# Optimization experiments

Hardware: AMD Instinct MI355X
Metric: run time of the kernel (lower is better)

The kernel has to match this reference:

```python
import jax, jax.numpy as jnp
import numpy as np

N, D_TOK, K = 8192, 256, 16


def knn_idx(xyz, k):
    # squared pairwise distances, diagonal excluded (loop=False)
    sq = jnp.sum(xyz * xyz, axis=-1)                      # [N]
    dist = sq[:, None] - 2.0 * (xyz @ xyz.T) + sq[None, :]  # [N,N]
    dist = dist + jnp.eye(xyz.shape[0], dtype=xyz.dtype) * jnp.asarray(1e10, xyz.dtype)
    _, idx = jax.lax.top_k(-dist, k)                      # [N,k] nearest neighbors j for each target i
    return idx


def edgeconv(x, nbr, W1, b1, W2, b2):
    # EdgeConv message: nn(concat(x_i, x_j - x_i)), aggr = max over neighbors
    n, d = x.shape
    k = nbr.shape[1]
    xi = x[:, None, :]                                    # [N,1,D]
    xj = x[nbr]                                           # [N,k,D] gather
    msg = jnp.concatenate([jnp.broadcast_to(xi, (n, k, d)), xj - xi], axis=-1)  # [N,k,2D]
    h = jax.nn.relu(msg @ W1 + b1) @ W2 + b2              # [N,k,token_dim]
    return jnp.max(h, axis=1)                             # [N,token_dim]


def setup_inputs() -> dict:
    key = jax.random.key(0)
    ks = jax.random.split(key, 10)
    d_in = 2 * (D_TOK + 3)
    s1 = 1.0 / np.sqrt(d_in)
    s2 = 1.0 / np.sqrt(D_TOK)
    return {
        "xyz": jax.random.normal(ks[0], (N, 3), dtype=jnp.float32),
        "feat": jax.random.normal(ks[1], (N, D_TOK), dtype=jnp.float32),
        "W1a": jax.random.normal(ks[2], (d_in, D_TOK), dtype=jnp.float32) * s1,
        "b1a": jnp.zeros((D_TOK,), dtype=jnp.float32),
        "W2a": jax.random.normal(ks[3], (D_TOK, D_TOK), dtype=jnp.float32) * s2,
        "b2a": jnp.zeros((D_TOK,), dtype=jnp.float32),
        "W1b": jax.random.normal(ks[4], (d_in, D_TOK), dtype=jnp.float32) * s1,
        "b1b": jnp.zeros((D_TOK,), dtype=jnp.float32),
        "W2b": jax.random.normal(ks[5], (D_TOK, D_TOK), dtype=jnp.float32) * s2,
        "b2b": jnp.zeros((D_TOK,), dtype=jnp.float32),
    }


def reference(xyz, feat, W1a, b1a, W2a, b2a, W1b, b1b, W2b, b2b):
    nbr = knn_idx(xyz, K)                                 # [N,k], built once, reused by both convs
    x = jnp.concatenate([feat, xyz], axis=-1)             # [N, D_TOK+3]
    x = edgeconv(x, nbr, W1a, b1a, W2a, b2a)              # [N, D_TOK]
    x = jnp.concatenate([x, xyz], axis=-1)                # [N, D_TOK+3]
    x = edgeconv(x, nbr, W1b, b1b, W2b, b2b)              # [N, D_TOK]
    return x
```

## Files before the change

kernel.cpp:

```cpp
#include <hip/hip_runtime.h>
#include <cfloat>

#define N_PTS 8192
#define DTOK 256
#define KNN 16

typedef __attribute__((ext_vector_type(8))) short short8;
typedef __attribute__((ext_vector_type(4))) float float4v;
typedef __attribute__((ext_vector_type(2))) float float2v;

__device__ inline short f2bf(float f) {
  unsigned u = __float_as_uint(f);
  u += 0x7fffu + ((u >> 16) & 1u);
  return (short)(u >> 16);
}
__device__ inline float bf2f(short h) {
  return __uint_as_float(((unsigned)(unsigned short)h) << 16);
}

__device__ inline float2v pk_mul(float2v a, float2v b) {
  float2v d;
  asm("v_pk_mul_f32 %0, %1, %2" : "=v"(d) : "v"(a), "v"(b));
  return d;
}
__device__ inline float2v pk_fma(float2v a, float2v b, float2v c) {
  float2v d;
  asm("v_pk_fma_f32 %0, %1, %2, %3" : "=v"(d) : "v"(a), "v"(b), "v"(c));
  return d;
}
__device__ inline float2v pk_add(float2v a, float2v b) {
  float2v d;
  asm("v_pk_add_f32 %0, %1, %2" : "=v"(d) : "v"(a), "v"(b));
  return d;
}

__global__ __launch_bounds__(256) void knn_prep_kernel(
    const float* __restrict__ xyz, float4* __restrict__ xyz4) {
  const int i = blockIdx.x * 256 + threadIdx.x;
  float x = xyz[3 * i], y = xyz[3 * i + 1], z = xyz[3 * i + 2];
  float sq = __fadd_rn(__fadd_rn(__fmul_rn(x, x), __fmul_rn(y, y)),
                       __fmul_rn(z, z));
  xyz4[i] = make_float4(x, y, z, sq);
}

__device__ inline void insert_group(float d, int base, float t, int lane,
                                    float& sd, int& sj, float& s15) {
  unsigned long long m = __ballot(d <= t);
  while (m) {
    const int src = __ffsll(m) - 1;
    m &= m - 1;
    const float dc = __shfl(d, src);
    if (dc < s15) {
      const int jc = base + src;
      const unsigned long long bm = __ballot(sd <= dc) & 0xFFFFull;
      const int pos = (int)__popcll(bm);
      const float pu = __shfl_up(sd, 1);
      const int ju = __shfl_up(sj, 1);
      if (lane < 16) {
        if (lane > pos)        { sd = pu; sj = ju; }
        else if (lane == pos)  { sd = dc; sj = jc; }
      }
      s15 = __shfl(sd, 15);
    }
  }
}

#define KCH 512
#define NCH (N_PTS / KCH)

__global__ __launch_bounds__(256) void knn_select_kernel(
    const float4* __restrict__ xyz4, int* __restrict__ nbr) {
  __shared__ float4 sA[2][4][64];
  __shared__ float4 sB[2][4][64];
  const int tid = threadIdx.x;
  const int lane = tid & 63;
  const int wave = tid >> 6;
  const int i0 = blockIdx.x * 8 + wave * 2;
  const int i1 = i0 + 1;

  const float4 q0 = xyz4[i0];
  const float4 q1 = xyz4[i1];
  const float2v x02 = {q0.x, q0.x}, y02 = {q0.y, q0.y};
  const float2v z02 = {q0.z, q0.z}, s02 = {q0.w, q0.w};
  const float2v x12 = {q1.x, q1.x}, y12 = {q1.y, q1.y};
  const float2v z12 = {q1.z, q1.z}, s12 = {q1.w, q1.w};
  const float2v n2 = {-2.0f, -2.0f};

  const int ib128 = i0 & ~127;
  const int ih0 = (i0 >> 6) & 1, il0 = i0 & 63;
  const int ih1 = (i1 >> 6) & 1, il1 = i1 & 63;

  const int sgj = wave * 128 + lane;

  {
    const float4 c0 = xyz4[sgj];
    const float4 c1 = xyz4[sgj + 64];
    sA[0][wave][lane] = make_float4(c0.x, c1.x, c0.y, c1.y);
    sB[0][wave][lane] = make_float4(c0.z, c1.z, c0.w, c1.w);
  }
  __syncthreads();

  float a00 = FLT_MAX, a01 = FLT_MAX, a10 = FLT_MAX, a11 = FLT_MAX;
  for (int c = 0; c < NCH; ++c) {
    const int b = c & 1;
    float4 nx0, nx1;
    if (c < NCH - 1) {
      nx0 = xyz4[(c + 1) * KCH + sgj];
      nx1 = xyz4[(c + 1) * KCH + sgj + 64];
    }
    const int cbase = c * KCH;
    #pragma unroll
    for (int ps = 0; ps < 4; ++ps) {
      const float4 a = sA[b][ps][lane];
      const float4 bb = sB[b][ps][lane];
      const float2v px = {a.x, a.y}, py = {a.z, a.w};
      const float2v pz = {bb.x, bb.y}, pw = {bb.z, bb.w};
      const bool selfg = (cbase + ps * 128 == ib128);
      const float2v dot0 =
          pk_fma(z02, pz, pk_fma(y02, py, pk_mul(x02, px)));
      float2v d0 = pk_add(pk_fma(n2, dot0, s02), pw);
      const float2v dot1 =
          pk_fma(z12, pz, pk_fma(y12, py, pk_mul(x12, px)));
      float2v d1 = pk_add(pk_fma(n2, dot1, s12), pw);
      if (selfg) {
        if (lane == il0) {
          if (ih0) d0.y = __fadd_rn(d0.y, 1e10f);
          else     d0.x = __fadd_rn(d0.x, 1e10f);
        }
        if (lane == il1) {
          if (ih1) d1.y = __fadd_rn(d1.y, 1e10f);
          else     d1.x = __fadd_rn(d1.x, 1e10f);
        }
      }
      a00 = fminf(a00, d0.x);
      a01 = fminf(a01, d0.y);
      a10 = fminf(a10, d1.x);
      a11 = fminf(a11, d1.y);
    }
    if (c < NCH - 1) {
      sA[b ^ 1][wave][lane] = make_float4(nx0.x, nx1.x, nx0.y, nx1.y);
      sB[b ^ 1][wave][lane] = make_float4(nx0.z, nx1.z, nx0.w, nx1.w);
    }
    __syncthreads();
  }

  float v0 = fminf(a00, a01);
  float v1 = fminf(a10, a11);
  #pragma unroll
  for (int k = 2; k <= 64; k <<= 1) {
    #pragma unroll
    for (int j = k >> 1; j > 0; j >>= 1) {
      const float o0 = __shfl_xor(v0, j, 64);
      const float o1 = __shfl_xor(v1, j, 64);
      const bool keepmin = ((lane & k) == 0) == ((lane & j) == 0);
      v0 = keepmin ? fminf(v0, o0) : fmaxf(v0, o0);
      v1 = keepmin ? fminf(v1, o1) : fmaxf(v1, o1);
    }
  }
  const float t0 = __shfl(v0, 15, 64);
  const float t1 = __shfl(v1, 15, 64);

  float sd0 = FLT_MAX, sd1 = FLT_MAX;
  int sj0 = 0, sj1 = 0;
  float s150 = FLT_MAX, s151 = FLT_MAX;

  const int gself = i0 >> 6;

  float4 pc = xyz4[lane];
  #pragma unroll 2
  for (int grp = 0; grp < N_PTS / 64; ++grp) {
    float4 pn;
    if (grp < N_PTS / 64 - 1) pn = xyz4[(grp + 1) * 64 + lane];

    const float dot0 = fmaf(q0.z, pc.z, fmaf(q0.y, pc.y,
                                             __fmul_rn(q0.x, pc.x)));
    float d0 = __fadd_rn(__fmaf_rn(-2.0f, dot0, q0.w), pc.w);
    const float dot1 = fmaf(q1.z, pc.z, fmaf(q1.y, pc.y,
                                             __fmul_rn(q1.x, pc.x)));
    float d1 = __fadd_rn(__fmaf_rn(-2.0f, dot1, q1.w), pc.w);
    if (grp == gself) {
      if (lane == il0) d0 = __fadd_rn(d0, 1e10f);
      if (lane == il1) d1 = __fadd_rn(d1, 1e10f);
    }

    insert_group(d0, grp * 64, t0, lane, sd0, sj0, s150);
    insert_group(d1, grp * 64, t1, lane, sd1, sj1, s151);
    pc = pn;
  }

  if (lane < 16) {
    nbr[i0 * KNN + lane] = sj0;
    nbr[i1 * KNN + lane] = sj1;
  }
}

__global__ __launch_bounds__(256) void convert_w_kernel(
    const float* __restrict__ W1, short* __restrict__ bhi,
    short* __restrict__ blo) {
  const int n = blockIdx.x;
  const int k = threadIdx.x;
  const float v = (n < 256) ? W1[k * DTOK + n]
                            : W1[(259 + k) * DTOK + (n - 256)];
  short h = f2bf(v);
  bhi[n * 256 + k] = h;
  blo[n * 256 + k] = f2bf(v - bf2f(h));
}

__global__ __launch_bounds__(256, 2) void pq_gemm_fused_kernel(
    const float* __restrict__ A, const short* __restrict__ Bthi,
    const short* __restrict__ Btlo, const float* __restrict__ xyz,
    const float* __restrict__ W1, const float* __restrict__ b1,
    float* __restrict__ R, float* __restrict__ Q) {
  __shared__ short Ahi[64][32], Alo[64][32];
  __shared__ short Bhi[128][32], Blo[128][32];
  __shared__ float Qs[64][65];
  __shared__ float sx[64][3];
  __shared__ float swz[6][64];
  __shared__ float sb1[64];

  const int tid = threadIdx.x;
  const int lane = tid & 63;
  const int wave = tid >> 6;
  const int l15 = lane & 15;
  const int quad = lane >> 4;
  const int mh = wave & 1;
  const int qh = wave >> 1;
  const int m0 = blockIdx.x * 64;
  const int np0 = blockIdx.y * 64;

  if (tid < 64) {
    sx[tid][0] = xyz[(m0 + tid) * 3];
    sx[tid][1] = xyz[(m0 + tid) * 3 + 1];
    sx[tid][2] = xyz[(m0 + tid) * 3 + 2];
  } else if (tid < 128) {
    int n = tid - 64;
    sb1[n] = b1[np0 + n];
    #pragma unroll
    for (int r = 0; r < 3; ++r) {
      swz[r][n] = W1[(256 + r) * DTOK + np0 + n];
      swz[3 + r][n] = W1[(515 + r) * DTOK + np0 + n];
    }
  }

  float4v acc[2][4];
  #pragma unroll
  for (int mf = 0; mf < 2; ++mf)
    #pragma unroll
    for (int nf = 0; nf < 4; ++nf)
      #pragma unroll
      for (int e = 0; e < 4; ++e) acc[mf][nf][e] = 0.f;

  const int ar = tid >> 2;
  const int ak = (tid & 3) * 8;

  #pragma unroll 1
  for (int kc = 0; kc < 8; ++kc) {
    const int k0 = kc * 32;
    __syncthreads();
    {
      const float* asrc = A + (size_t)(m0 + ar) * 256 + k0 + ak;
      float4 a0 = *(const float4*)asrc;
      float4 a1 = *(const float4*)(asrc + 4);
      float v[8] = {a0.x, a0.y, a0.z, a0.w, a1.x, a1.y, a1.z, a1.w};
      short8 h8, l8;
      #pragma unroll
      for (int e = 0; e < 8; ++e) {
        short h = f2bf(v[e]);
        h8[e] = h;
        l8[e] = f2bf(v[e] - bf2f(h));
      }
      *(short8*)(&Ahi[ar][ak]) = h8;
      *(short8*)(&Alo[ar][ak]) = l8;
    }
    #pragma unroll
    for (int l = 0; l < 4; ++l) {
      const int rem = tid + 256 * (l & 1);
      const int row = rem >> 2;
      const int koff = (rem & 3) * 8;
      const int n = (row < 64) ? (np0 + row) : (256 + np0 + row - 64);
      const short* src = ((l < 2) ? Bthi : Btlo) + (size_t)n * 256 + k0 + koff;
      short8 vv = *(const short8*)src;
      if (l < 2) *(short8*)(&Bhi[row][koff]) = vv;
      else       *(short8*)(&Blo[row][koff]) = vv;
    }
    __syncthreads();

    short8 ah[2], al[2], bh[4], bl[4];
    #pragma unroll
    for (int mf = 0; mf < 2; ++mf) {
      ah[mf] = *(const short8*)(&Ahi[mh * 32 + mf * 16 + l15][quad * 8]);
      al[mf] = *(const short8*)(&Alo[mh * 32 + mf * 16 + l15][quad * 8]);
    }
    #pragma unroll
    for (int nf = 0; nf < 4; ++nf) {
      bh[nf] = *(const short8*)(&Bhi[qh * 64 + nf * 16 + l15][quad * 8]);
      bl[nf] = *(const short8*)(&Blo[qh * 64 + nf * 16 + l15][quad * 8]);
    }
    #pragma unroll
    for (int mf = 0; mf < 2; ++mf)
      #pragma unroll
      for (int nf = 0; nf < 4; ++nf) {
        acc[mf][nf] = __builtin_amdgcn_mfma_f32_16x16x32_bf16(
            ah[mf], bh[nf], acc[mf][nf], 0, 0, 0);
        acc[mf][nf] = __builtin_amdgcn_mfma_f32_16x16x32_bf16(
            ah[mf], bl[nf], acc[mf][nf], 0, 0, 0);
        acc[mf][nf] = __builtin_amdgcn_mfma_f32_16x16x32_bf16(
            al[mf], bh[nf], acc[mf][nf], 0, 0, 0);
      }
  }

  if (qh == 1) {
    #pragma unroll
    for (int mf = 0; mf < 2; ++mf)
      #pragma unroll
      for (int nf = 0; nf < 4; ++nf)
        #pragma unroll
        for (int e = 0; e < 4; ++e) {
          int row = mh * 32 + mf * 16 + quad * 4 + e;
          int col = nf * 16 + l15;
          float q = acc[mf][nf][e] + sx[row][0] * swz[3][col] +
                    sx[row][1] * swz[4][col] + sx[row][2] * swz[5][col];
          Qs[row][col] = q;
          Q[(size_t)(m0 + row) * DTOK + np0 + col] = q;
        }
  }
  __syncthreads();
  if (qh == 0) {
    #pragma unroll
    for (int mf = 0; mf < 2; ++mf)
      #pragma unroll
      for (int nf = 0; nf < 4; ++nf)
        #pragma unroll
        for (int e = 0; e < 4; ++e) {
          int row = mh * 32 + mf * 16 + quad * 4 + e;
          int col = nf * 16 + l15;
          float p = acc[mf][nf][e] + sx[row][0] * swz[0][col] +
                    sx[row][1] * swz[1][col] + sx[row][2] * swz[2][col];
          R[(size_t)(m0 + row) * DTOK + np0 + col] =
              (p + sb1[col]) - Qs[row][col];
        }
  }
}

#define EP 8

__global__ __launch_bounds__(256, 2) void edge_mfma_kernel(
    const float* __restrict__ R, const float* __restrict__ Q,
    const int* __restrict__ nbr, const float* __restrict__ W2,
    const float* __restrict__ b2, float* __restrict__ out,
    int num_groups, int groups_per_block) {
  __shared__ short Hs[EP * KNN * DTOK];
  const int lane = threadIdx.x & 63;
  const int wave = threadIdx.x >> 6;
  const int l15 = lane & 15;
  const int quad = lane >> 4;

  short8 bfr[4][8];
  #pragma unroll
  for (int nt_i = 0; nt_i < 4; ++nt_i) {
    const int n = (wave * 4 + nt_i) * 16 + l15;
    #pragma unroll
    for (int kt = 0; kt < 8; ++kt) {
      short8 f;
      #pragma unroll
      for (int jj = 0; jj < 8; ++jj) {
        int k = kt * 32 + quad * 8 + jj;
        f[jj] = f2bf(W2[k * DTOK + n]);
      }
      bfr[nt_i][kt] = f;
    }
  }

  const int wc8 = lane >> 1;
  const int wsub = (lane & 1) * 4;

  for (int gi = 0; gi < groups_per_block; ++gi) {
    const int g = blockIdx.x + gi * gridDim.x;
    if (g >= num_groups) break;
    const int i0 = g * EP;

    {
      const int ia = i0 + wave * 2;
      const int jr0 = nbr[ia * KNN + l15];
      const int jr1 = nbr[(ia + 1) * KNN + l15];
      const float4 ri0 = ((const float4*)(R + (size_t)ia * DTOK))[lane];
      const float4 ri1 = ((const float4*)(R + (size_t)(ia + 1) * DTOK))[lane];
      #pragma unroll
      for (int pp = 0; pp < 2; ++pp) {
        const float4 ri = pp ? ri1 : ri0;
        const int jr = pp ? jr1 : jr0;
        #pragma unroll
        for (int k = 0; k < KNN; ++k) {
          const int j = __shfl(jr, k, 16);
          const float4 qj = ((const float4*)(Q + (size_t)j * DTOK))[lane];
          const int r = wave * 32 + pp * 16 + k;
          uint2 pk;
          pk.x = ((unsigned)(unsigned short)f2bf(fmaxf(ri.x + qj.x, 0.f))) |
                 (((unsigned)(unsigned short)f2bf(fmaxf(ri.y + qj.y, 0.f))) << 16);
          pk.y = ((unsigned)(unsigned short)f2bf(fmaxf(ri.z + qj.z, 0.f))) |
                 (((unsigned)(unsigned short)f2bf(fmaxf(ri.w + qj.w, 0.f))) << 16);
          *(uint2*)(&Hs[r * DTOK + ((wc8 ^ (r & 7)) << 3) + wsub]) = pk;
        }
      }
    }
    __syncthreads();

    #pragma unroll
    for (int mp = 0; mp < 4; ++mp) {
      float4v acc[2][4];
      #pragma unroll
      for (int mi = 0; mi < 2; ++mi)
        #pragma unroll
        for (int nt_i = 0; nt_i < 4; ++nt_i)
          #pragma unroll
          for (int e = 0; e < 4; ++e) acc[mi][nt_i][e] = 0.f;

      #pragma unroll
      for (int kt = 0; kt < 8; ++kt) {
        const int pc = ((kt * 4 + quad) ^ (l15 & 7)) << 3;
        const short8 a0 = *(const short8*)(
            &Hs[((mp * 2 + 0) * 16 + l15) * DTOK + pc]);
        const short8 a1 = *(const short8*)(
            &Hs[((mp * 2 + 1) * 16 + l15) * DTOK + pc]);
        #pragma unroll
        for (int nt_i = 0; nt_i < 4; ++nt_i) {
          acc[0][nt_i] = __builtin_amdgcn_mfma_f32_16x16x32_bf16(
              a0, bfr[nt_i][kt], acc[0][nt_i], 0, 0, 0);
          acc[1][nt_i] = __builtin_amdgcn_mfma_f32_16x16x32_bf16(
              a1, bfr[nt_i][kt], acc[1][nt_i], 0, 0, 0);
        }
      }

      #pragma unroll
      for (int mi = 0; mi < 2; ++mi) {
        #pragma unroll
        for (int nt_i = 0; nt_i < 4; ++nt_i) {
          float rm = fmaxf(fmaxf(acc[mi][nt_i][0], acc[mi][nt_i][1]),
                           fmaxf(acc[mi][nt_i][2], acc[mi][nt_i][3]));
          rm = fmaxf(rm, __shfl_xor(rm, 16, 64));
          rm = fmaxf(rm, __shfl_xor(rm, 32, 64));
          if (lane < 16) {
            const int i = i0 + mp * 2 + mi;
            const int n = (wave * 4 + nt_i) * 16 + lane;
            out[(size_t)i * DTOK + n] = rm + b2[n];
          }
        }
      }
    }
    __syncthreads();
  }
}

extern "C" void kernel_launch(void* const* d_in, const int* in_sizes, int n_in,
                              void* d_out, int out_size, void* d_ws,
                              size_t ws_size, hipStream_t stream) {
  const float* xyz = (const float*)d_in[0];
  const float* feat = (const float*)d_in[1];
  const float* W1a = (const float*)d_in[2];
  const float* b1a = (const float*)d_in[3];
  const float* W2a = (const float*)d_in[4];
  const float* b2a = (const float*)d_in[5];
  const float* W1b = (const float*)d_in[6];
  const float* b1b = (const float*)d_in[7];
  const float* W2b = (const float*)d_in[8];
  const float* b2b = (const float*)d_in[9];
  float* out = (float*)d_out;

  char* w = (char*)d_ws;
  const size_t SZ_NBR = (size_t)N_PTS * KNN * sizeof(int);
  const size_t MB = 1024 * 1024;
  int* nbr = (int*)w;
  char* w1 = w + SZ_NBR;
  float4* xyz4 = (float4*)w1;
  float* R = (float*)(w1 + 8 * MB);
  float* Q = (float*)(w + SZ_NBR + 16 * MB);
  short* Bthi = (short*)(w + SZ_NBR + 24 * MB);
  short* Btlo = Bthi + 512 * 256;
  float* bufC = out;

  knn_prep_kernel<<<N_PTS / 256, 256, 0, stream>>>(xyz, xyz4);
  knn_select_kernel<<<N_PTS / 8, 256, 0, stream>>>(xyz4, nbr);

  const int num_groups = N_PTS / EP;
  const int nblocks = 512;

  convert_w_kernel<<<512, 256, 0, stream>>>(W1a, Bthi, Btlo);
  pq_gemm_fused_kernel<<<dim3(N_PTS / 64, 4), 256, 0, stream>>>(
      feat, Bthi, Btlo, xyz, W1a, b1a, R, Q);
  edge_mfma_kernel<<<nblocks, 256, 0, stream>>>(R, Q, nbr, W2a, b2a, bufC,
                                                num_groups, 2);

  convert_w_kernel<<<512, 256, 0, stream>>>(W1b, Bthi, Btlo);
  pq_gemm_fused_kernel<<<dim3(N_PTS / 64, 4), 256, 0, stream>>>(
      bufC, Bthi, Btlo, xyz, W1b, b1b, R, Q);
  edge_mfma_kernel<<<nblocks, 256, 0, stream>>>(R, Q, nbr, W2b, b2b, out,
                                                num_groups, 2);
}
```

Measured before the change: 229.7 us.

## Fuse kNN selection and first P/Q GEMM into one heterogeneous kernel launch

```diff
diff --git a/kernel.cpp b/kernel.cpp
--- a/kernel.cpp
+++ b/kernel.cpp
@@ -65,135 +65,6 @@
   }
 }
 
-#define KCH 512
-#define NCH (N_PTS / KCH)
-
-__global__ __launch_bounds__(256) void knn_select_kernel(
-    const float4* __restrict__ xyz4, int* __restrict__ nbr) {
-  __shared__ float4 sA[2][4][64];
-  __shared__ float4 sB[2][4][64];
-  const int tid = threadIdx.x;
-  const int lane = tid & 63;
-  const int wave = tid >> 6;
-  const int i0 = blockIdx.x * 8 + wave * 2;
-  const int i1 = i0 + 1;
-
-  const float4 q0 = xyz4[i0];
-  const float4 q1 = xyz4[i1];
-  const float2v x02 = {q0.x, q0.x}, y02 = {q0.y, q0.y};
-  const float2v z02 = {q0.z, q0.z}, s02 = {q0.w, q0.w};
-  const float2v x12 = {q1.x, q1.x}, y12 = {q1.y, q1.y};
-  const float2v z12 = {q1.z, q1.z}, s12 = {q1.w, q1.w};
-  const float2v n2 = {-2.0f, -2.0f};
-
-  const int ib128 = i0 & ~127;
-  const int ih0 = (i0 >> 6) & 1, il0 = i0 & 63;
-  const int ih1 = (i1 >> 6) & 1, il1 = i1 & 63;
-
-  const int sgj = wave * 128 + lane;
-
-  {
-    const float4 c0 = xyz4[sgj];
-    const float4 c1 = xyz4[sgj + 64];
-    sA[0][wave][lane] = make_float4(c0.x, c1.x, c0.y, c1.y);
-    sB[0][wave][lane] = make_float4(c0.z, c1.z, c0.w, c1.w);
-  }
-  __syncthreads();
-
-  float a00 = FLT_MAX, a01 = FLT_MAX, a10 = FLT_MAX, a11 = FLT_MAX;
-  for (int c = 0; c < NCH; ++c) {
-    const int b = c & 1;
-    float4 nx0, nx1;
-    if (c < NCH - 1) {
-      nx0 = xyz4[(c + 1) * KCH + sgj];
-      nx1 = xyz4[(c + 1) * KCH + sgj + 64];
-    }
-    const int cbase = c * KCH;
-    #pragma unroll
-    for (int ps = 0; ps < 4; ++ps) {
-      const float4 a = sA[b][ps][lane];
-      const float4 bb = sB[b][ps][lane];
-      const float2v px = {a.x, a.y}, py = {a.z, a.w};
-      const float2v pz = {bb.x, bb.y}, pw = {bb.z, bb.w};
-      const bool selfg = (cbase + ps * 128 == ib128);
-      const float2v dot0 =
-          pk_fma(z02, pz, pk_fma(y02, py, pk_mul(x02, px)));
-      float2v d0 = pk_add(pk_fma(n2, dot0, s02), pw);
-      const float2v dot1 =
-          pk_fma(z12, pz, pk_fma(y12, py, pk_mul(x12, px)));
-      float2v d1 = pk_add(pk_fma(n2, dot1, s12), pw);
-      if (selfg) {
-        if (lane == il0) {
-          if (ih0) d0.y = __fadd_rn(d0.y, 1e10f);
-          else     d0.x = __fadd_rn(d0.x, 1e10f);
-        }
-        if (lane == il1) {
-          if (ih1) d1.y = __fadd_rn(d1.y, 1e10f);
-          else     d1.x = __fadd_rn(d1.x, 1e10f);
-        }
-      }
-      a00 = fminf(a00, d0.x);
-      a01 = fminf(a01, d0.y);
-      a10 = fminf(a10, d1.x);
-      a11 = fminf(a11, d1.y);
-    }
-    if (c < NCH - 1) {
-      sA[b ^ 1][wave][lane] = make_float4(nx0.x, nx1.x, nx0.y, nx1.y);
-      sB[b ^ 1][wave][lane] = make_float4(nx0.z, nx1.z, nx0.w, nx1.w);
-    }
-    __syncthreads();
-  }
-
-  float v0 = fminf(a00, a01);
-  float v1 = fminf(a10, a11);
-  #pragma unroll
-  for (int k = 2; k <= 64; k <<= 1) {
-    #pragma unroll
-    for (int j = k >> 1; j > 0; j >>= 1) {
-      const float o0 = __shfl_xor(v0, j, 64);
-      const float o1 = __shfl_xor(v1, j, 64);
-      const bool keepmin = ((lane & k) == 0) == ((lane & j) == 0);
-      v0 = keepmin ? fminf(v0, o0) : fmaxf(v0, o0);
-      v1 = keepmin ? fminf(v1, o1) : fmaxf(v1, o1);
-    }
-  }
-  const float t0 = __shfl(v0, 15, 64);
-  const float t1 = __shfl(v1, 15, 64);
-
-  float sd0 = FLT_MAX, sd1 = FLT_MAX;
-  int sj0 = 0, sj1 = 0;
-  float s150 = FLT_MAX, s151 = FLT_MAX;
-
-  const int gself = i0 >> 6;
-
-  float4 pc = xyz4[lane];
-  #pragma unroll 2
-  for (int grp = 0; grp < N_PTS / 64; ++grp) {
-    float4 pn;
-    if (grp < N_PTS / 64 - 1) pn = xyz4[(grp + 1) * 64 + lane];
-
-    const float dot0 = fmaf(q0.z, pc.z, fmaf(q0.y, pc.y,
-                                             __fmul_rn(q0.x, pc.x)));
-    float d0 = __fadd_rn(__fmaf_rn(-2.0f, dot0, q0.w), pc.w);
-    const float dot1 = fmaf(q1.z, pc.z, fmaf(q1.y, pc.y,
-                                             __fmul_rn(q1.x, pc.x)));
-    float d1 = __fadd_rn(__fmaf_rn(-2.0f, dot1, q1.w), pc.w);
-    if (grp == gself) {
-      if (lane == il0) d0 = __fadd_rn(d0, 1e10f);
-      if (lane == il1) d1 = __fadd_rn(d1, 1e10f);
-    }
-
-    insert_group(d0, grp * 64, t0, lane, sd0, sj0, s150);
-    insert_group(d1, grp * 64, t1, lane, sd1, sj1, s151);
-    pc = pn;
-  }
-
-  if (lane < 16) {
-    nbr[i0 * KNN + lane] = sj0;
-    nbr[i1 * KNN + lane] = sj1;
-  }
-}
-
 __global__ __launch_bounds__(256) void convert_w_kernel(
     const float* __restrict__ W1, short* __restrict__ bhi,
     short* __restrict__ blo) {
@@ -204,6 +75,280 @@
   short h = f2bf(v);
   bhi[n * 256 + k] = h;
   blo[n * 256 + k] = f2bf(v - bf2f(h));
+}
+
+#define KCH 512
+#define NCH (N_PTS / KCH)
+
+__global__ __launch_bounds__(256, 2) void knn_gemm_fused_kernel(
+    const float4* __restrict__ xyz4, int* __restrict__ nbr,
+    const float* __restrict__ A, const short* __restrict__ Bthi,
+    const short* __restrict__ Btlo, const float* __restrict__ xyz,
+    const float* __restrict__ W1, const float* __restrict__ b1,
+    float* __restrict__ R, float* __restrict__ Q) {
+  __shared__ __align__(16) char smem[27136];
+
+  const int bid = blockIdx.x;
+  const int tid = threadIdx.x;
+  const int lane = tid & 63;
+  const int wave = tid >> 6;
+  const int l15 = lane & 15;
+  const int quad = lane >> 4;
+
+  if (bid % 3 != 2) {
+    float4 (*sA)[4][64] = (float4 (*)[4][64])(smem);
+    float4 (*sB)[4][64] = (float4 (*)[4][64])(smem + 8192);
+
+    const int kb = (bid / 3) * 2 + (bid % 3);
+    const int i0 = kb * 8 + wave * 2;
+    const int i1 = i0 + 1;
+
+    const float4 q0 = xyz4[i0];
+    const float4 q1 = xyz4[i1];
+    const float2v x02 = {q0.x, q0.x}, y02 = {q0.y, q0.y};
+    const float2v z02 = {q0.z, q0.z}, s02 = {q0.w, q0.w};
+    const float2v x12 = {q1.x, q1.x}, y12 = {q1.y, q1.y};
+    const float2v z12 = {q1.z, q1.z}, s12 = {q1.w, q1.w};
+    const float2v n2 = {-2.0f, -2.0f};
+
+    const int ib128 = i0 & ~127;
+    const int ih0 = (i0 >> 6) & 1, il0 = i0 & 63;
+    const int ih1 = (i1 >> 6) & 1, il1 = i1 & 63;
+
+    const int sgj = wave * 128 + lane;
+
+    {
+      const float4 c0 = xyz4[sgj];
+      const float4 c1 = xyz4[sgj + 64];
+      sA[0][wave][lane] = make_float4(c0.x, c1.x, c0.y, c1.y);
+      sB[0][wave][lane] = make_float4(c0.z, c1.z, c0.w, c1.w);
+    }
+    __syncthreads();
+
+    float a00 = FLT_MAX, a01 = FLT_MAX, a10 = FLT_MAX, a11 = FLT_MAX;
+    for (int c = 0; c < NCH; ++c) {
+      const int b = c & 1;
+      float4 nx0, nx1;
+      if (c < NCH - 1) {
+        nx0 = xyz4[(c + 1) * KCH + sgj];
+        nx1 = xyz4[(c + 1) * KCH + sgj + 64];
+      }
+      const int cbase = c * KCH;
+      #pragma unroll
+      for (int ps = 0; ps < 4; ++ps) {
+        const float4 a = sA[b][ps][lane];
+        const float4 bb = sB[b][ps][lane];
+        const float2v px = {a.x, a.y}, py = {a.z, a.w};
+        const float2v pz = {bb.x, bb.y}, pw = {bb.z, bb.w};
+        const bool selfg = (cbase + ps * 128 == ib128);
+        const float2v dot0 =
+            pk_fma(z02, pz, pk_fma(y02, py, pk_mul(x02, px)));
+        float2v d0 = pk_add(pk_fma(n2, dot0, s02), pw);
+        const float2v dot1 =
+            pk_fma(z12, pz, pk_fma(y12, py, pk_mul(x12, px)));
+        float2v d1 = pk_add(pk_fma(n2, dot1, s12), pw);
+        if (selfg) {
+          if (lane == il0) {
+            if (ih0) d0.y = __fadd_rn(d0.y, 1e10f);
+            else     d0.x = __fadd_rn(d0.x, 1e10f);
+          }
+          if (lane == il1) {
+            if (ih1) d1.y = __fadd_rn(d1.y, 1e10f);
+            else     d1.x = __fadd_rn(d1.x, 1e10f);
+          }
+        }
+        a00 = fminf(a00, d0.x);
+        a01 = fminf(a01, d0.y);
+        a10 = fminf(a10, d1.x);
+        a11 = fminf(a11, d1.y);
+      }
+      if (c < NCH - 1) {
+        sA[b ^ 1][wave][lane] = make_float4(nx0.x, nx1.x, nx0.y, nx1.y);
+        sB[b ^ 1][wave][lane] = make_float4(nx0.z, nx1.z, nx0.w, nx1.w);
+      }
+      __syncthreads();
+    }
+
+    float v0 = fminf(a00, a01);
+    float v1 = fminf(a10, a11);
+    #pragma unroll
+    for (int k = 2; k <= 64; k <<= 1) {
+      #pragma unroll
+      for (int j = k >> 1; j > 0; j >>= 1) {
+        const float o0 = __shfl_xor(v0, j, 64);
+        const float o1 = __shfl_xor(v1, j, 64);
+        const bool keepmin = ((lane & k) == 0) == ((lane & j) == 0);
+        v0 = keepmin ? fminf(v0, o0) : fmaxf(v0, o0);
+        v1 = keepmin ? fminf(v1, o1) : fmaxf(v1, o1);
+      }
+    }
+    const float t0 = __shfl(v0, 15, 64);
+    const float t1 = __shfl(v1, 15, 64);
+
+    float sd0 = FLT_MAX, sd1 = FLT_MAX;
+    int sj0 = 0, sj1 = 0;
+    float s150 = FLT_MAX, s151 = FLT_MAX;
+
+    const int gself = i0 >> 6;
+
+    float4 pc = xyz4[lane];
+    #pragma unroll 2
+    for (int grp = 0; grp < N_PTS / 64; ++grp) {
+      float4 pn;
+      if (grp < N_PTS / 64 - 1) pn = xyz4[(grp + 1) * 64 + lane];
+
+      const float dot0 = fmaf(q0.z, pc.z, fmaf(q0.y, pc.y,
+                                               __fmul_rn(q0.x, pc.x)));
+      float d0 = __fadd_rn(__fmaf_rn(-2.0f, dot0, q0.w), pc.w);
+      const float dot1 = fmaf(q1.z, pc.z, fmaf(q1.y, pc.y,
+                                               __fmul_rn(q1.x, pc.x)));
+      float d1 = __fadd_rn(__fmaf_rn(-2.0f, dot1, q1.w), pc.w);
+      if (grp == gself) {
+        if (lane == il0) d0 = __fadd_rn(d0, 1e10f);
+        if (lane == il1) d1 = __fadd_rn(d1, 1e10f);
+      }
+
+      insert_group(d0, grp * 64, t0, lane, sd0, sj0, s150);
+      insert_group(d1, grp * 64, t1, lane, sd1, sj1, s151);
+      pc = pn;
+    }
+
+    if (lane < 16) {
+      nbr[i0 * KNN + lane] = sj0;
+      nbr[i1 * KNN + lane] = sj1;
+    }
+    return;
+  }
+
+  short (*Ahi)[32] = (short (*)[32])(smem);
+  short (*Alo)[32] = (short (*)[32])(smem + 4096);
+  short (*Bhi)[32] = (short (*)[32])(smem + 8192);
+  short (*Blo)[32] = (short (*)[32])(smem + 16384);
+  float (*Qs)[65]  = (float (*)[65])(smem);
+  float (*sx)[3]   = (float (*)[3])(smem + 24576);
+  float (*swz)[64] = (float (*)[64])(smem + 25344);
+  float* sb1       = (float*)(smem + 26880);
+
+  const int g = bid / 3;
+  const int m0 = (g >> 2) * 64;
+  const int np0 = (g & 3) * 64;
+  const int mh = wave & 1;
+  const int qh = wave >> 1;
+
+  if (tid < 64) {
+    sx[tid][0] = xyz[(m0 + tid) * 3];
+    sx[tid][1] = xyz[(m0 + tid) * 3 + 1];
+    sx[tid][2] = xyz[(m0 + tid) * 3 + 2];
+  } else if (tid < 128) {
+    int n = tid - 64;
+    sb1[n] = b1[np0 + n];
+    #pragma unroll
+    for (int r = 0; r < 3; ++r) {
+      swz[r][n] = W1[(256 + r) * DTOK + np0 + n];
+      swz[3 + r][n] = W1[(515 + r) * DTOK + np0 + n];
+    }
+  }
+
+  float4v acc[2][4];
+  #pragma unroll
+  for (int mf = 0; mf < 2; ++mf)
+    #pragma unroll
+    for (int nf = 0; nf < 4; ++nf)
+      #pragma unroll
+      for (int e = 0; e < 4; ++e) acc[mf][nf][e] = 0.f;
+
+  const int ar = tid >> 2;
+  const int ak = (tid & 3) * 8;
+
+  #pragma unroll 1
+  for (int kc = 0; kc < 8; ++kc) {
+    const int k0 = kc * 32;
+    __syncthreads();
+    {
+      const float* asrc = A + (size_t)(m0 + ar) * 256 + k0 + ak;
+      float4 a0 = *(const float4*)asrc;
+      float4 a1 = *(const float4*)(asrc + 4);
+      float v[8] = {a0.x, a0.y, a0.z, a0.w, a1.x, a1.y, a1.z, a1.w};
+      short8 h8, l8;
+      #pragma unroll
+      for (int e = 0; e < 8; ++e) {
+        short h = f2bf(v[e]);
+        h8[e] = h;
+        l8[e] = f2bf(v[e] - bf2f(h));
+      }
+      *(short8*)(&Ahi[ar][ak]) = h8;
+      *(short8*)(&Alo[ar][ak]) = l8;
+    }
+    #pragma unroll
+    for (int l = 0; l < 4; ++l) {
+      const int rem = tid + 256 * (l & 1);
+      const int row = rem >> 2;
+      const int koff = (rem & 3) * 8;
+      const int n = (row < 64) ? (np0 + row) : (256 + np0 + row - 64);
+      const short* src = ((l < 2) ? Bthi : Btlo) + (size_t)n * 256 + k0 + koff;
+      short8 vv = *(const short8*)src;
+      if (l < 2) *(short8*)(&Bhi[row][koff]) = vv;
+      else       *(short8*)(&Blo[row][koff]) = vv;
+    }
+    __syncthreads();
+
+    short8 ah[2], al[2], bh[4], bl[4];
+    #pragma unroll
+    for (int mf = 0; mf < 2; ++mf) {
+      ah[mf] = *(const short8*)(&Ahi[mh * 32 + mf * 16 + l15][quad * 8]);
+      al[mf] = *(const short8*)(&Alo[mh * 32 + mf * 16 + l15][quad * 8]);
+    }
+    #pragma unroll
+    for (int nf = 0; nf < 4; ++nf) {
+      bh[nf] = *(const short8*)(&Bhi[qh * 64 + nf * 16 + l15][quad * 8]);
+      bl[nf] = *(const short8*)(&Blo[qh * 64 + nf * 16 + l15][quad * 8]);
+    }
+    #pragma unroll
+    for (int mf = 0; mf < 2; ++mf)
+      #pragma unroll
+      for (int nf = 0; nf < 4; ++nf) {
+        acc[mf][nf] = __builtin_amdgcn_mfma_f32_16x16x32_bf16(
+            ah[mf], bh[nf], acc[mf][nf], 0, 0, 0);
+        acc[mf][nf] = __builtin_amdgcn_mfma_f32_16x16x32_bf16(
+            ah[mf], bl[nf], acc[mf][nf], 0, 0, 0);
+        acc[mf][nf] = __builtin_amdgcn_mfma_f32_16x16x32_bf16(
+            al[mf], bh[nf], acc[mf][nf], 0, 0, 0);
+      }
+  }
+
+  __syncthreads();
+
+  if (qh == 1) {
+    #pragma unroll
+    for (int mf = 0; mf < 2; ++mf)
+      #pragma unroll
+      for (int nf = 0; nf < 4; ++nf)
+        #pragma unroll
+        for (int e = 0; e < 4; ++e) {
+          int row = mh * 32 + mf * 16 + quad * 4 + e;
+          int col = nf * 16 + l15;
+          float q = acc[mf][nf][e] + sx[row][0] * swz[3][col] +
+                    sx[row][1] * swz[4][col] + sx[row][2] * swz[5][col];
+          Qs[row][col] = q;
+          Q[(size_t)(m0 + row) * DTOK + np0 + col] = q;
+        }
+  }
+  __syncthreads();
+  if (qh == 0) {
+    #pragma unroll
+    for (int mf = 0; mf < 2; ++mf)
+      #pragma unroll
+      for (int nf = 0; nf < 4; ++nf)
+        #pragma unroll
+        for (int e = 0; e < 4; ++e) {
+          int row = mh * 32 + mf * 16 + quad * 4 + e;
+          int col = nf * 16 + l15;
+          float p = acc[mf][nf][e] + sx[row][0] * swz[0][col] +
+                    sx[row][1] * swz[1][col] + sx[row][2] * swz[2][col];
+          R[(size_t)(m0 + row) * DTOK + np0 + col] =
+              (p + sb1[col]) - Qs[row][col];
+        }
+  }
 }
 
 __global__ __launch_bounds__(256, 2) void pq_gemm_fused_kernel(
@@ -479,14 +624,13 @@
   float* bufC = out;
 
   knn_prep_kernel<<<N_PTS / 256, 256, 0, stream>>>(xyz, xyz4);
-  knn_select_kernel<<<N_PTS / 8, 256, 0, stream>>>(xyz4, nbr);
 
   const int num_groups = N_PTS / EP;
   const int nblocks = 512;
 
   convert_w_kernel<<<512, 256, 0, stream>>>(W1a, Bthi, Btlo);
-  pq_gemm_fused_kernel<<<dim3(N_PTS / 64, 4), 256, 0, stream>>>(
-      feat, Bthi, Btlo, xyz, W1a, b1a, R, Q);
+  knn_gemm_fused_kernel<<<1536, 256, 0, stream>>>(
+      xyz4, nbr, feat, Bthi, Btlo, xyz, W1a, b1a, R, Q);
   edge_mfma_kernel<<<nblocks, 256, 0, stream>>>(R, Q, nbr, W2a, b2a, bufC,
                                                 num_groups, 2);
 
```

After: 239.8 us. 1.04x slower.
